# Kernel tuning notes

Hardware: AMD Instinct MI355X
Metric: run time of the kernel (lower is better)

The kernel has to match this reference:

```python
import jax, jax.numpy as jnp
import numpy as np
from jax import lax

KERNEL = 3
STRIDE = 2
PADDING = 1


def setup_inputs() -> dict:
    key = jax.random.key(0)
    x = jax.random.normal(key, (2, 32, 128, 128, 128), dtype=jnp.float32)
    return {"x": x}


def reference(x):
    # Equivalent to: pad D/H/W with -inf by PADDING, then windowed max with
    # KERNEL window and STRIDE stride over the last three dims.
    # lax.reduce_window with -inf init and explicit padding reproduces this exactly.
    return lax.reduce_window(
        x,
        -jnp.inf,
        lax.max,
        window_dimensions=(1, 1, KERNEL, KERNEL, KERNEL),
        window_strides=(1, 1, STRIDE, STRIDE, STRIDE),
        padding=[(0, 0), (0, 0), (PADDING, PADDING), (PADDING, PADDING), (PADDING, PADDING)],
    )
```

## Files before the change

### kernel.cpp

```cpp
#include <hip/hip_runtime.h>
#include <math.h>


#define D_IN 128
#define H_IN 128
#define W_IN 128
#define D_OUT 64
#define H_OUT 64
#define W_OUT 64
#define NC 64

__device__ __forceinline__ float4 fmax4(float4 a, float4 b) {
    return make_float4(fmaxf(a.x, b.x), fmaxf(a.y, b.y), fmaxf(a.z, b.z), fmaxf(a.w, b.w));
}

__global__ __launch_bounds__(256) void maxpool3d_k3s2p1_v3(const float* __restrict__ x,
                                                           float* __restrict__ out) {
    const int t  = threadIdx.x & 31;
    const int hy = threadIdx.x >> 5;
    const int h_out0 = blockIdx.x * 16 + hy * 2;
    const int k0     = blockIdx.y * 16;
    const int nc     = blockIdx.z;

    const int h_in0 = 2 * h_out0 - 1;
    const bool h0ok = (h_in0 >= 0);

    const float* __restrict__ base =
        x + (size_t)nc * (D_IN * H_IN * W_IN) + (ptrdiff_t)h_in0 * W_IN + 4 * t;
    float* __restrict__ obase =
        out + ((size_t)nc * D_OUT) * (H_OUT * W_OUT) + (size_t)h_out0 * W_OUT + 2 * t;

    auto planeMax = [&](int d) -> float4 {
        const float* p = base + (size_t)d * (H_IN * W_IN);
        float rwx[5], rwy[5];
#pragma unroll
        for (int r = 0; r < 5; ++r) {
            float4 v;
            if (r == 0 && !h0ok) {
                v = make_float4(-INFINITY, -INFINITY, -INFINITY, -INFINITY);
            } else {
                v = *reinterpret_cast<const float4*>(p + r * W_IN);
            }
            float left = __shfl_up(v.w, 1, 64);
            if (t == 0) left = -INFINITY;
            rwx[r] = fmaxf(left, fmaxf(v.x, v.y));
            rwy[r] = fmaxf(v.y, fmaxf(v.z, v.w));
        }
        float4 ph;
        ph.x = fmaxf(rwx[0], fmaxf(rwx[1], rwx[2]));
        ph.y = fmaxf(rwy[0], fmaxf(rwy[1], rwy[2]));
        ph.z = fmaxf(rwx[2], fmaxf(rwx[3], rwx[4]));
        ph.w = fmaxf(rwy[2], fmaxf(rwy[3], rwy[4]));
        return ph;
    };

    auto storeK = [&](int k, float4 o) {
        float* orow = obase + (size_t)k * (H_OUT * W_OUT);
        *reinterpret_cast<float2*>(orow) = make_float2(o.x, o.y);
        *reinterpret_cast<float2*>(orow + W_OUT) = make_float2(o.z, o.w);
    };

    float4 acc;
    if (k0 == 0) {
        acc = planeMax(0);
    } else {
        acc = fmax4(planeMax(2 * k0 - 1), planeMax(2 * k0));
    }

#pragma unroll 2
    for (int i = 0; i < 15; ++i) {
        const int k = k0 + i;
        const float4 v1 = planeMax(2 * k + 1);
        storeK(k, fmax4(acc, v1));
        const float4 v2 = planeMax(2 * k + 2);
        acc = fmax4(v1, v2);
    }
    const int kl = k0 + 15;
    storeK(kl, fmax4(acc, planeMax(2 * kl + 1)));
}

extern "C" void kernel_launch(void* const* d_in, const int* in_sizes, int n_in,
                              void* d_out, int out_size, void* d_ws, size_t ws_size,
                              hipStream_t stream) {
    const float* x = (const float*)d_in[0];
    float* out = (float*)d_out;
    dim3 grid(H_OUT / 16, 4, NC);
    dim3 block(256);
    maxpool3d_k3s2p1_v3<<<grid, block, 0, stream>>>(x, out);
}
```

Measured before the change: 124.3 us.

## Double-buffer plane loads, halve depth per block, use nontemporal stores

Result: faster. 118.2 us (-4.9%).

```diff
diff --git a/kernel.cpp b/kernel.cpp
--- a/kernel.cpp
+++ b/kernel.cpp
@@ -5,78 +5,105 @@
 #define D_IN 128
 #define H_IN 128
 #define W_IN 128
+#define HW (H_IN * W_IN)
 #define D_OUT 64
 #define H_OUT 64
 #define W_OUT 64
 #define NC 64
+#define KPB 8
+
+typedef float vf2 __attribute__((ext_vector_type(2)));
+
+struct P5 { float4 r0, r1, r2, r3, r4; };
 
 __device__ __forceinline__ float4 fmax4(float4 a, float4 b) {
     return make_float4(fmaxf(a.x, b.x), fmaxf(a.y, b.y), fmaxf(a.z, b.z), fmaxf(a.w, b.w));
 }
 
-__global__ __launch_bounds__(256) void maxpool3d_k3s2p1_v3(const float* __restrict__ x,
+__device__ __forceinline__ P5 loadPlane(const float* __restrict__ p, int r0off) {
+    P5 v;
+    v.r0 = *reinterpret_cast<const float4*>(p + r0off);
+    v.r1 = *reinterpret_cast<const float4*>(p + W_IN);
+    v.r2 = *reinterpret_cast<const float4*>(p + 2 * W_IN);
+    v.r3 = *reinterpret_cast<const float4*>(p + 3 * W_IN);
+    v.r4 = *reinterpret_cast<const float4*>(p + 4 * W_IN);
+    return v;
+}
+
+__device__ __forceinline__ float rowL(float4 v, int t) {
+    float left = __shfl_up(v.w, 1, 64);
+    if (t == 0) left = -INFINITY;
+    return fmaxf(left, fmaxf(v.x, v.y));
+}
+__device__ __forceinline__ float rowR(float4 v) {
+    return fmaxf(v.y, fmaxf(v.z, v.w));
+}
+
+__device__ __forceinline__ float4 poolPlane(const P5& v, int t, bool h0ok) {
+    float ax0 = rowL(v.r0, t), ay0 = rowR(v.r0);
+    if (!h0ok) { ax0 = -INFINITY; ay0 = -INFINITY; }
+    float ax1 = rowL(v.r1, t), ay1 = rowR(v.r1);
+    float ax2 = rowL(v.r2, t), ay2 = rowR(v.r2);
+    float ax3 = rowL(v.r3, t), ay3 = rowR(v.r3);
+    float ax4 = rowL(v.r4, t), ay4 = rowR(v.r4);
+    float4 o;
+    o.x = fmaxf(ax0, fmaxf(ax1, ax2));
+    o.y = fmaxf(ay0, fmaxf(ay1, ay2));
+    o.z = fmaxf(ax2, fmaxf(ax3, ax4));
+    o.w = fmaxf(ay2, fmaxf(ay3, ay4));
+    return o;
+}
+
+__global__ __launch_bounds__(256) void maxpool3d_k3s2p1_v4(const float* __restrict__ x,
                                                            float* __restrict__ out) {
     const int t  = threadIdx.x & 31;
     const int hy = threadIdx.x >> 5;
     const int h_out0 = blockIdx.x * 16 + hy * 2;
-    const int k0     = blockIdx.y * 16;
+    const int k0     = blockIdx.y * KPB;
     const int nc     = blockIdx.z;
 
     const int h_in0 = 2 * h_out0 - 1;
     const bool h0ok = (h_in0 >= 0);
+    const int r0off = h0ok ? 0 : W_IN;
 
     const float* __restrict__ base =
-        x + (size_t)nc * (D_IN * H_IN * W_IN) + (ptrdiff_t)h_in0 * W_IN + 4 * t;
+        x + (size_t)nc * (D_IN * HW) + (ptrdiff_t)h_in0 * W_IN + 4 * t;
     float* __restrict__ obase =
-        out + ((size_t)nc * D_OUT) * (H_OUT * W_OUT) + (size_t)h_out0 * W_OUT + 2 * t;
-
-    auto planeMax = [&](int d) -> float4 {
-        const float* p = base + (size_t)d * (H_IN * W_IN);
-        float rwx[5], rwy[5];
-#pragma unroll
-        for (int r = 0; r < 5; ++r) {
-            float4 v;
-            if (r == 0 && !h0ok) {
-                v = make_float4(-INFINITY, -INFINITY, -INFINITY, -INFINITY);
-            } else {
-                v = *reinterpret_cast<const float4*>(p + r * W_IN);
-            }
-            float left = __shfl_up(v.w, 1, 64);
-            if (t == 0) left = -INFINITY;
-            rwx[r] = fmaxf(left, fmaxf(v.x, v.y));
-            rwy[r] = fmaxf(v.y, fmaxf(v.z, v.w));
-        }
-        float4 ph;
-        ph.x = fmaxf(rwx[0], fmaxf(rwx[1], rwx[2]));
-        ph.y = fmaxf(rwy[0], fmaxf(rwy[1], rwy[2]));
-        ph.z = fmaxf(rwx[2], fmaxf(rwx[3], rwx[4]));
-        ph.w = fmaxf(rwy[2], fmaxf(rwy[3], rwy[4]));
-        return ph;
-    };
+        out + (size_t)nc * (D_OUT * H_OUT * W_OUT) + (size_t)h_out0 * W_OUT + 2 * t;
 
     auto storeK = [&](int k, float4 o) {
         float* orow = obase + (size_t)k * (H_OUT * W_OUT);
-        *reinterpret_cast<float2*>(orow) = make_float2(o.x, o.y);
-        *reinterpret_cast<float2*>(orow + W_OUT) = make_float2(o.z, o.w);
+        vf2 lo = {o.x, o.y}, hi = {o.z, o.w};
+        __builtin_nontemporal_store(lo, reinterpret_cast<vf2*>(orow));
+        __builtin_nontemporal_store(hi, reinterpret_cast<vf2*>(orow + W_OUT));
     };
 
+    P5 A, B;
     float4 acc;
     if (k0 == 0) {
-        acc = planeMax(0);
+        A = loadPlane(base, r0off);
+        P5 A1 = loadPlane(base + HW, r0off);
+        acc = poolPlane(A, t, h0ok);
+        A = A1;
     } else {
-        acc = fmax4(planeMax(2 * k0 - 1), planeMax(2 * k0));
+        A = loadPlane(base + (size_t)(2 * k0 - 1) * HW, r0off);
+        B = loadPlane(base + (size_t)(2 * k0) * HW, r0off);
+        float4 a0 = poolPlane(A, t, h0ok);
+        A = loadPlane(base + (size_t)(2 * k0 + 1) * HW, r0off);
+        acc = fmax4(a0, poolPlane(B, t, h0ok));
     }
 
-#pragma unroll 2
-    for (int i = 0; i < 15; ++i) {
-        const int k = k0 + i;
-        const float4 v1 = planeMax(2 * k + 1);
+#pragma unroll 1
+    for (int k = k0; k < k0 + KPB - 1; ++k) {
+        B = loadPlane(base + (size_t)(2 * k + 2) * HW, r0off);
+        float4 v1 = poolPlane(A, t, h0ok);
         storeK(k, fmax4(acc, v1));
-        const float4 v2 = planeMax(2 * k + 2);
+        A = loadPlane(base + (size_t)(2 * k + 3) * HW, r0off);
+        float4 v2 = poolPlane(B, t, h0ok);
         acc = fmax4(v1, v2);
     }
-    const int kl = k0 + 15;
-    storeK(kl, fmax4(acc, planeMax(2 * kl + 1)));
+    const int kl = k0 + KPB - 1;
+    storeK(kl, fmax4(acc, poolPlane(A, t, h0ok)));
 }
 
 extern "C" void kernel_launch(void* const* d_in, const int* in_sizes, int n_in,
@@ -84,7 +111,7 @@
                               hipStream_t stream) {
     const float* x = (const float*)d_in[0];
     float* out = (float*)d_out;
-    dim3 grid(H_OUT / 16, 4, NC);
+    dim3 grid(H_OUT / 16, D_OUT / KPB, NC);
     dim3 block(256);
-    maxpool3d_k3s2p1_v3<<<grid, block, 0, stream>>>(x, out);
+    maxpool3d_k3s2p1_v4<<<grid, block, 0, stream>>>(x, out);
 }
```
